# Kernel tuning notes

Measured on AMD Instinct MI355X. Metric: run time of the kernel, lower is better.

Reference implementation:

```python
import jax, jax.numpy as jnp
import numpy as np

EPS = 1e-12  # torch F.normalize eps

def _l2norm(v, axis):
    return v / jnp.maximum(jnp.linalg.norm(v, axis=axis, keepdims=True), EPS)

def setup_inputs() -> dict:
    key = jax.random.key(0)
    k1, k2, k3 = jax.random.split(key, 3)
    N, C, H, W, K = 128, 64, 64, 64, 100
    ALPHA = 100.0
    x = jax.random.normal(k1, (N, C, H, W), dtype=jnp.float32)
    # centroids initialized as F.normalize(rand(K, C)) per __init__
    centroids = jax.random.uniform(k2, (K, C), dtype=jnp.float32)
    centroids = _l2norm(centroids, axis=1)
    # _init_params ties conv weight/bias to centroids (random=False)
    conv_w = 2.0 * ALPHA * centroids                      # [K, C] (1x1 conv kernel)
    conv_b = -ALPHA * jnp.linalg.norm(centroids, axis=1)  # [K]
    return {"x": x, "conv_w": conv_w, "conv_b": conv_b, "centroids": centroids}

def reference(x, conv_w, conv_b, centroids):
    N, C, H, W = x.shape
    K = centroids.shape[0]
    xf = x.reshape(N, C, H * W)                      # [N, C, L]
    # get_assignments: L2-normalize over channels (local copy only)
    x_hat = _l2norm(xf, axis=1)
    logits = jnp.einsum('kc,ncl->nkl', conv_w, x_hat) + conv_b[None, :, None]
    a = jax.nn.softmax(logits, axis=1)               # soft assignment over K
    # residual sum over L expressed as matmul (same math as expand-subtract-sum):
    # vlad[n,k,c] = sum_l a[n,k,l]*xf[n,c,l] - centroids[k,c]*sum_l a[n,k,l]
    agg = jnp.einsum('nkl,ncl->nkc', a, xf)          # note: un-normalized xf, per original code
    vlad = agg - centroids[None] * jnp.sum(a, axis=-1)[..., None]
    # build_vlad (random=False): intra-normalize per cluster, flatten, L2-normalize
    vlad = _l2norm(vlad, axis=2)
    vlad = vlad.reshape(N, K * C)
    vlad = _l2norm(vlad, axis=1)
    # Wrapper applies a final F.normalize (idempotent here but kept for faithfulness)
    vlad = _l2norm(vlad, axis=1)
    return vlad
```

## Files before the change

### kernel.cpp

```cpp
#include <hip/hip_runtime.h>
#include <hip/hip_bf16.h>
#include <cstdint>

#define NB   128
#define CD   64
#define LD   4096
#define KC   100
#define KT   7
#define KR   (KT * 16)
#define AKP  72
#define LSPLIT 8
#define LCH  (LD / LSPLIT)
#define ITERS (LCH / 64)

typedef __attribute__((ext_vector_type(8))) short bf16x8;
typedef __attribute__((ext_vector_type(4))) float f32x4;

__device__ __forceinline__ short bfbits(float f) {
    __hip_bfloat16 h = __float2bfloat16(f);
    return *reinterpret_cast<short*>(&h);
}
__device__ __forceinline__ float bffloat(short s) {
    __hip_bfloat16 h = *reinterpret_cast<__hip_bfloat16*>(&s);
    return __bfloat162float(h);
}

__global__ void k_prep(const float* __restrict__ w, const float* __restrict__ b,
                       uint4* __restrict__ wfrag, float* __restrict__ b_pad)
{
    const int tid = threadIdx.x;
    if (tid < 128) b_pad[tid] = (tid < KC) ? b[tid] : -1e30f;
    if (tid < 64) {
        const int r16 = tid & 15, gg = tid >> 4;
        for (int t = 0; t < KT; ++t) {
            const int k = t * 16 + r16;
            for (int h = 0; h < 2; ++h) {
                short hi8[8], lo8[8];
                for (int j = 0; j < 8; ++j) {
                    const int c = h * 32 + gg * 8 + j;
                    float v = (k < KC) ? w[k * CD + c] : 0.f;
                    short hb = bfbits(v);
                    hi8[j] = hb;
                    lo8[j] = bfbits(v - bffloat(hb));
                }
                wfrag[((t * 2 + h) * 2 + 0) * 64 + tid] = *reinterpret_cast<uint4*>(hi8);
                wfrag[((t * 2 + h) * 2 + 1) * 64 + tid] = *reinterpret_cast<uint4*>(lo8);
            }
        }
    }
}

__global__ __launch_bounds__(256, 3) void k_fused(
    const float* __restrict__ x, const uint4* __restrict__ wfrag,
    const float* __restrict__ b_pad,
    float* __restrict__ agg_pT, float* __restrict__ asum_pT, int n0)
{
    __shared__ __align__(16) __hip_bfloat16 akl[KR][AKP];
    __shared__ __align__(16) uint4 wlds[KT * 2 * 2 * 64];

    const int tid  = threadIdx.x;
    const int lane = tid & 63;
    const int wv   = tid >> 6;
    const int lloc = lane & 15;
    const int g    = lane >> 4;

    for (int i = tid; i < KT * 2 * 2 * 64; i += 256) wlds[i] = wfrag[i];

    const int nn = blockIdx.x >> 3;
    const int ls = blockIdx.x & 7;
    const int n  = n0 + nn;
    const float* xb = x + (size_t)n * CD * LD + ls * LCH;

    const float4* bp4 = reinterpret_cast<const float4*>(b_pad);
    float4 bv[KT];
#pragma unroll
    for (int t = 0; t < KT; ++t) bv[t] = bp4[t * 4 + g];

    f32x4 aagg[KT];
#pragma unroll
    for (int mt = 0; mt < KT; ++mt) aagg[mt] = (f32x4){0.f, 0.f, 0.f, 0.f};
    float asl = 0.f;

    const bf16x8* wfp = reinterpret_cast<const bf16x8*>(wlds);
    const int lw = wv * 16 + lloc;
    const int cb = wv * 16 + lloc;

    __syncthreads();

    for (int it = 0; it < ITERS; ++it) {
        const float* xcol = xb + it * 64 + lw;
        float ss = 0.f;
        bf16x8 bhi0, blo0, bhi1, blo1;
#pragma unroll
        for (int j = 0; j < 8; ++j) {
            float v0 = xcol[(size_t)(g * 8 + j) * LD];
            ss = fmaf(v0, v0, ss);
            short h0 = bfbits(v0);
            bhi0[j] = h0; blo0[j] = bfbits(v0 - bffloat(h0));
            float v1 = xcol[(size_t)(32 + g * 8 + j) * LD];
            ss = fmaf(v1, v1, ss);
            short h1 = bfbits(v1);
            bhi1[j] = h1; blo1[j] = bfbits(v1 - bffloat(h1));
        }
        ss += __shfl_xor(ss, 16);
        ss += __shfl_xor(ss, 32);
        const float rn = 1.0f / fmaxf(sqrtf(ss), 1e-12f);

        f32x4 acc[KT];
#pragma unroll
        for (int t = 0; t < KT; ++t) acc[t] = (f32x4){0.f, 0.f, 0.f, 0.f};
#pragma unroll
        for (int t = 0; t < KT; ++t) {
            bf16x8 wh0 = wfp[((t * 2 + 0) * 2 + 0) * 64 + lane];
            bf16x8 wl0 = wfp[((t * 2 + 0) * 2 + 1) * 64 + lane];
            bf16x8 wh1 = wfp[((t * 2 + 1) * 2 + 0) * 64 + lane];
            bf16x8 wl1 = wfp[((t * 2 + 1) * 2 + 1) * 64 + lane];
            acc[t] = __builtin_amdgcn_mfma_f32_16x16x32_bf16(wh0, bhi0, acc[t], 0, 0, 0);
            acc[t] = __builtin_amdgcn_mfma_f32_16x16x32_bf16(wh1, bhi1, acc[t], 0, 0, 0);
            acc[t] = __builtin_amdgcn_mfma_f32_16x16x32_bf16(wh0, blo0, acc[t], 0, 0, 0);
            acc[t] = __builtin_amdgcn_mfma_f32_16x16x32_bf16(wh1, blo1, acc[t], 0, 0, 0);
            acc[t] = __builtin_amdgcn_mfma_f32_16x16x32_bf16(wl0, bhi0, acc[t], 0, 0, 0);
            acc[t] = __builtin_amdgcn_mfma_f32_16x16x32_bf16(wl1, bhi1, acc[t], 0, 0, 0);
        }

        float m = -3.0e38f;
#pragma unroll
        for (int t = 0; t < KT; ++t) {
            acc[t][0] = fmaf(acc[t][0], rn, bv[t].x);
            acc[t][1] = fmaf(acc[t][1], rn, bv[t].y);
            acc[t][2] = fmaf(acc[t][2], rn, bv[t].z);
            acc[t][3] = fmaf(acc[t][3], rn, bv[t].w);
            m = fmaxf(m, fmaxf(fmaxf(acc[t][0], acc[t][1]), fmaxf(acc[t][2], acc[t][3])));
        }
        m = fmaxf(m, __shfl_xor(m, 16));
        m = fmaxf(m, __shfl_xor(m, 32));
        float s = 0.f;
#pragma unroll
        for (int t = 0; t < KT; ++t) {
#pragma unroll
            for (int r = 0; r < 4; ++r) {
                float e = __expf(acc[t][r] - m);
                acc[t][r] = e;
                s += e;
            }
        }
        s += __shfl_xor(s, 16);
        s += __shfl_xor(s, 32);
        const float inv = 1.0f / s;

        __syncthreads();

#pragma unroll
        for (int r = 0; r < 4; ++r) {
#pragma unroll
            for (int t = 0; t < KT; ++t)
                akl[t * 16 + g * 4 + r][lw] = __float2bfloat16(acc[t][r] * inv);
        }
        __syncthreads();

        if (tid < KR) {
            const bf16x8* rp = reinterpret_cast<const bf16x8*>(&akl[tid][0]);
            float rs = 0.f;
#pragma unroll
            for (int q = 0; q < 8; ++q) {
                bf16x8 v = rp[q];
#pragma unroll
                for (int j = 0; j < 8; ++j) rs += bffloat(v[j]);
            }
            asl += rs;
        }

#pragma unroll
        for (int h = 0; h < 2; ++h) {
            const float* xrow = xb + (size_t)cb * LD + it * 64 + h * 32 + g * 8;
            float4 xr0 = *reinterpret_cast<const float4*>(xrow);
            float4 xr1 = *reinterpret_cast<const float4*>(xrow + 4);
            float xv8[8] = {xr0.x, xr0.y, xr0.z, xr0.w, xr1.x, xr1.y, xr1.z, xr1.w};
            bf16x8 xh, xl;
#pragma unroll
            for (int j = 0; j < 8; ++j) {
                float v = xv8[j];
                short hb = bfbits(v);
                xh[j] = hb; xl[j] = bfbits(v - bffloat(hb));
            }
#pragma unroll
            for (int mt = 0; mt < KT; ++mt) {
                bf16x8 af = *reinterpret_cast<const bf16x8*>(
                    &akl[mt * 16 + lloc][h * 32 + g * 8]);
                aagg[mt] = __builtin_amdgcn_mfma_f32_16x16x32_bf16(af, xh, aagg[mt], 0, 0, 0);
                aagg[mt] = __builtin_amdgcn_mfma_f32_16x16x32_bf16(af, xl, aagg[mt], 0, 0, 0);
            }
        }
    }

    const size_t nls = (size_t)nn * LSPLIT + ls;
    float* ap = agg_pT + (nls * 64 + cb) * 128 + g * 4;
#pragma unroll
    for (int mt = 0; mt < KT; ++mt)
        *reinterpret_cast<f32x4*>(ap + mt * 16) = aagg[mt];
    if (tid < KR) asum_pT[nls * KR + tid] = asl;
}

__global__ __launch_bounds__(256, 1) void k_final(
    const float* __restrict__ agg_pT, const float* __restrict__ asum_pT,
    const float* __restrict__ cent, float* __restrict__ out, int n0)
{
    __shared__ float vbuf[KC][65];
    __shared__ float asum_s[KR];
    __shared__ float rn_s[KC];
    __shared__ float red[256];

    const int tid = threadIdx.x;
    const int nn  = blockIdx.x;
    const int n   = n0 + nn;
    const size_t nb8 = (size_t)nn * LSPLIT;

    if (tid < KR) {
        float s = 0.f;
#pragma unroll
        for (int ls = 0; ls < LSPLIT; ++ls)
            s += asum_pT[(nb8 + ls) * KR + tid];
        asum_s[tid] = s;
    }
    __syncthreads();

    for (int idx = tid; idx < 64 * 128; idx += 256) {
        int c = idx >> 7, k = idx & 127;
        if (k < KC) {
            float s = 0.f;
#pragma unroll
            for (int ls = 0; ls < LSPLIT; ++ls)
                s += agg_pT[((nb8 + ls) * 64 + c) * 128 + k];
            vbuf[k][c] = fmaf(-cent[k * CD + c], asum_s[k], s);
        }
    }
    __syncthreads();

    if (tid < KC) {
        float ssq = 0.f;
#pragma unroll 8
        for (int c = 0; c < CD; ++c) {
            float v = vbuf[tid][c];
            ssq = fmaf(v, v, ssq);
        }
        rn_s[tid] = 1.0f / fmaxf(sqrtf(ssq), 1e-12f);
    }
    __syncthreads();

    float gp = 0.f;
    for (int idx = tid; idx < KC * CD; idx += 256) {
        int k = idx >> 6, c = idx & 63;
        float v = vbuf[k][c] * rn_s[k];
        gp = fmaf(v, v, gp);
    }
    red[tid] = gp;
    __syncthreads();
    for (int off = 128; off > 0; off >>= 1) {
        if (tid < off) red[tid] += red[tid + off];
        __syncthreads();
    }
    const float gnorm = 1.0f / fmaxf(sqrtf(red[0]), 1e-12f);

    float* op = out + (size_t)n * (KC * CD);
    for (int idx = tid; idx < KC * CD; idx += 256) {
        int k = idx >> 6, c = idx & 63;
        op[idx] = vbuf[k][c] * rn_s[k] * gnorm;
    }
}

extern "C" void kernel_launch(void* const* d_in, const int* in_sizes, int n_in,
                              void* d_out, int out_size, void* d_ws, size_t ws_size,
                              hipStream_t stream)
{
    const float* x  = (const float*)d_in[0];
    const float* w  = (const float*)d_in[1];
    const float* b  = (const float*)d_in[2];
    const float* ct = (const float*)d_in[3];
    float* out = (float*)d_out;

    char* wsp = (char*)d_ws;
    uint4* wfrag = (uint4*)wsp;
    float* b_pad = (float*)(wsp + 28672);
    char* chunk  = wsp + 32768;

    const size_t agg_per_n  = (size_t)LSPLIT * 64 * 128 * 4;
    const size_t asum_per_n = (size_t)LSPLIT * KR * 4;
    const size_t per_n = agg_per_n + asum_per_n;

    size_t avail = ws_size > 32768 ? ws_size - 32768 : 0;
    int nc = (int)(avail / per_n);
    if (nc < 1) nc = 1;
    if (nc > NB) nc = NB;

    float* agg_pT  = (float*)chunk;
    float* asum_pT = (float*)(chunk + agg_per_n * (size_t)nc);

    k_prep<<<1, 128, 0, stream>>>(w, b, wfrag, b_pad);
    for (int n0 = 0; n0 < NB; n0 += nc) {
        int cn = NB - n0; if (cn > nc) cn = nc;
        k_fused<<<cn * LSPLIT, 256, 0, stream>>>(x, wfrag, b_pad, agg_pT, asum_pT, n0);
        k_final<<<cn, 256, 0, stream>>>(agg_pT, asum_pT, ct, out, n0);
    }
}
```

Baseline: 100.1 us.

## Prefetch next x tiles into registers and accumulate assignment sums in registers

Software-pipelines the global loads of x: the column and row fragments for the next 64-wide L chunk are issued into registers while the current chunk's softmax and aggregation MFMAs run. The per-iteration shared-memory row-sum of the assignment tile, done by a subset of threads, is replaced by per-lane fp32 partial sums reduced with shuffles and shared memory once at the end. Bias values are reloaded from global each iteration instead of held in registers to offset the extra prefetch registers. Register pressure rises under the 3-blocks-per-SM launch bound, which risks spills or lower occupancy. The assignment sums now come from fp32 values rather than the bf16-rounded tile, which slightly changes numerics.

```diff
diff --git a/kernel.cpp b/kernel.cpp
--- a/kernel.cpp
+++ b/kernel.cpp
@@ -57,6 +57,7 @@
 {
     __shared__ __align__(16) __hip_bfloat16 akl[KR][AKP];
     __shared__ __align__(16) uint4 wlds[KT * 2 * 2 * 64];
+    __shared__ float asum_sm[4][KR];
 
     const int tid  = threadIdx.x;
     const int lane = tid & 63;
@@ -72,32 +73,48 @@
     const float* xb = x + (size_t)n * CD * LD + ls * LCH;
 
     const float4* bp4 = reinterpret_cast<const float4*>(b_pad);
-    float4 bv[KT];
-#pragma unroll
-    for (int t = 0; t < KT; ++t) bv[t] = bp4[t * 4 + g];
 
     f32x4 aagg[KT];
 #pragma unroll
     for (int mt = 0; mt < KT; ++mt) aagg[mt] = (f32x4){0.f, 0.f, 0.f, 0.f};
-    float asl = 0.f;
+    float pasum[KT][4];
+#pragma unroll
+    for (int t = 0; t < KT; ++t)
+#pragma unroll
+        for (int r = 0; r < 4; ++r) pasum[t][r] = 0.f;
 
     const bf16x8* wfp = reinterpret_cast<const bf16x8*>(wlds);
     const int lw = wv * 16 + lloc;
     const int cb = wv * 16 + lloc;
 
+    float pvc[16];
+    float4 pvr0, pvr1, pvr2, pvr3;
+    {
+        const float* xcol = xb + lw;
+#pragma unroll
+        for (int j = 0; j < 8; ++j) {
+            pvc[j]     = xcol[(size_t)(g * 8 + j) * LD];
+            pvc[8 + j] = xcol[(size_t)(32 + g * 8 + j) * LD];
+        }
+        const float* xrow = xb + (size_t)cb * LD + g * 8;
+        pvr0 = *reinterpret_cast<const float4*>(xrow);
+        pvr1 = *reinterpret_cast<const float4*>(xrow + 4);
+        pvr2 = *reinterpret_cast<const float4*>(xrow + 32);
+        pvr3 = *reinterpret_cast<const float4*>(xrow + 36);
+    }
+
     __syncthreads();
 
     for (int it = 0; it < ITERS; ++it) {
-        const float* xcol = xb + it * 64 + lw;
         float ss = 0.f;
         bf16x8 bhi0, blo0, bhi1, blo1;
 #pragma unroll
         for (int j = 0; j < 8; ++j) {
-            float v0 = xcol[(size_t)(g * 8 + j) * LD];
+            float v0 = pvc[j];
             ss = fmaf(v0, v0, ss);
             short h0 = bfbits(v0);
             bhi0[j] = h0; blo0[j] = bfbits(v0 - bffloat(h0));
-            float v1 = xcol[(size_t)(32 + g * 8 + j) * LD];
+            float v1 = pvc[8 + j];
             ss = fmaf(v1, v1, ss);
             short h1 = bfbits(v1);
             bhi1[j] = h1; blo1[j] = bfbits(v1 - bffloat(h1));
@@ -126,10 +143,11 @@
         float m = -3.0e38f;
 #pragma unroll
         for (int t = 0; t < KT; ++t) {
-            acc[t][0] = fmaf(acc[t][0], rn, bv[t].x);
-            acc[t][1] = fmaf(acc[t][1], rn, bv[t].y);
-            acc[t][2] = fmaf(acc[t][2], rn, bv[t].z);
-            acc[t][3] = fmaf(acc[t][3], rn, bv[t].w);
+            float4 bt = bp4[t * 4 + g];
+            acc[t][0] = fmaf(acc[t][0], rn, bt.x);
+            acc[t][1] = fmaf(acc[t][1], rn, bt.y);
+            acc[t][2] = fmaf(acc[t][2], rn, bt.z);
+            acc[t][3] = fmaf(acc[t][3], rn, bt.w);
             m = fmaxf(m, fmaxf(fmaxf(acc[t][0], acc[t][1]), fmaxf(acc[t][2], acc[t][3])));
         }
         m = fmaxf(m, __shfl_xor(m, 16));
@@ -147,6 +165,14 @@
         s += __shfl_xor(s, 16);
         s += __shfl_xor(s, 32);
         const float inv = 1.0f / s;
+#pragma unroll
+        for (int t = 0; t < KT; ++t) {
+#pragma unroll
+            for (int r = 0; r < 4; ++r) {
+                acc[t][r] *= inv;
+                pasum[t][r] += acc[t][r];
+            }
+        }
 
         __syncthreads();
 
@@ -154,51 +180,73 @@
         for (int r = 0; r < 4; ++r) {
 #pragma unroll
             for (int t = 0; t < KT; ++t)
-                akl[t * 16 + g * 4 + r][lw] = __float2bfloat16(acc[t][r] * inv);
-        }
+                akl[t * 16 + g * 4 + r][lw] = __float2bfloat16(acc[t][r]);
+        }
+
+        if (it + 1 < ITERS) {
+            const float* xcol = xb + (it + 1) * 64 + lw;
+#pragma unroll
+            for (int j = 0; j < 8; ++j) {
+                pvc[j]     = xcol[(size_t)(g * 8 + j) * LD];
+                pvc[8 + j] = xcol[(size_t)(32 + g * 8 + j) * LD];
+            }
+        }
+
         __syncthreads();
 
-        if (tid < KR) {
-            const bf16x8* rp = reinterpret_cast<const bf16x8*>(&akl[tid][0]);
-            float rs = 0.f;
-#pragma unroll
-            for (int q = 0; q < 8; ++q) {
-                bf16x8 v = rp[q];
-#pragma unroll
-                for (int j = 0; j < 8; ++j) rs += bffloat(v[j]);
-            }
-            asl += rs;
-        }
-
-#pragma unroll
-        for (int h = 0; h < 2; ++h) {
-            const float* xrow = xb + (size_t)cb * LD + it * 64 + h * 32 + g * 8;
-            float4 xr0 = *reinterpret_cast<const float4*>(xrow);
-            float4 xr1 = *reinterpret_cast<const float4*>(xrow + 4);
-            float xv8[8] = {xr0.x, xr0.y, xr0.z, xr0.w, xr1.x, xr1.y, xr1.z, xr1.w};
-            bf16x8 xh, xl;
+        bf16x8 xh0, xl0, xh1, xl1;
+        {
+            float xv0[8] = {pvr0.x, pvr0.y, pvr0.z, pvr0.w, pvr1.x, pvr1.y, pvr1.z, pvr1.w};
+            float xv1[8] = {pvr2.x, pvr2.y, pvr2.z, pvr2.w, pvr3.x, pvr3.y, pvr3.z, pvr3.w};
 #pragma unroll
             for (int j = 0; j < 8; ++j) {
-                float v = xv8[j];
-                short hb = bfbits(v);
-                xh[j] = hb; xl[j] = bfbits(v - bffloat(hb));
-            }
-#pragma unroll
-            for (int mt = 0; mt < KT; ++mt) {
-                bf16x8 af = *reinterpret_cast<const bf16x8*>(
-                    &akl[mt * 16 + lloc][h * 32 + g * 8]);
-                aagg[mt] = __builtin_amdgcn_mfma_f32_16x16x32_bf16(af, xh, aagg[mt], 0, 0, 0);
-                aagg[mt] = __builtin_amdgcn_mfma_f32_16x16x32_bf16(af, xl, aagg[mt], 0, 0, 0);
-            }
-        }
-    }
+                short hb0 = bfbits(xv0[j]);
+                xh0[j] = hb0; xl0[j] = bfbits(xv0[j] - bffloat(hb0));
+                short hb1 = bfbits(xv1[j]);
+                xh1[j] = hb1; xl1[j] = bfbits(xv1[j] - bffloat(hb1));
+            }
+        }
+        if (it + 1 < ITERS) {
+            const float* xrow = xb + (size_t)cb * LD + (it + 1) * 64 + g * 8;
+            pvr0 = *reinterpret_cast<const float4*>(xrow);
+            pvr1 = *reinterpret_cast<const float4*>(xrow + 4);
+            pvr2 = *reinterpret_cast<const float4*>(xrow + 32);
+            pvr3 = *reinterpret_cast<const float4*>(xrow + 36);
+        }
+#pragma unroll
+        for (int mt = 0; mt < KT; ++mt) {
+            bf16x8 af0 = *reinterpret_cast<const bf16x8*>(&akl[mt * 16 + lloc][g * 8]);
+            aagg[mt] = __builtin_amdgcn_mfma_f32_16x16x32_bf16(af0, xh0, aagg[mt], 0, 0, 0);
+            aagg[mt] = __builtin_amdgcn_mfma_f32_16x16x32_bf16(af0, xl0, aagg[mt], 0, 0, 0);
+            bf16x8 af1 = *reinterpret_cast<const bf16x8*>(&akl[mt * 16 + lloc][32 + g * 8]);
+            aagg[mt] = __builtin_amdgcn_mfma_f32_16x16x32_bf16(af1, xh1, aagg[mt], 0, 0, 0);
+            aagg[mt] = __builtin_amdgcn_mfma_f32_16x16x32_bf16(af1, xl1, aagg[mt], 0, 0, 0);
+        }
+    }
+
+#pragma unroll
+    for (int t = 0; t < KT; ++t) {
+#pragma unroll
+        for (int r = 0; r < 4; ++r) {
+            float v = pasum[t][r];
+            v += __shfl_xor(v, 1);
+            v += __shfl_xor(v, 2);
+            v += __shfl_xor(v, 4);
+            v += __shfl_xor(v, 8);
+            if (lloc == 0) asum_sm[wv][t * 16 + g * 4 + r] = v;
+        }
+    }
+    __syncthreads();
 
     const size_t nls = (size_t)nn * LSPLIT + ls;
+    if (tid < KR)
+        asum_pT[nls * KR + tid] = asum_sm[0][tid] + asum_sm[1][tid]
+                                + asum_sm[2][tid] + asum_sm[3][tid];
+
     float* ap = agg_pT + (nls * 64 + cb) * 128 + g * 4;
 #pragma unroll
     for (int mt = 0; mt < KT; ++mt)
         *reinterpret_cast<f32x4*>(ap + mt * 16) = aagg[mt];
-    if (tid < KR) asum_pT[nls * KR + tid] = asl;
 }
 
 __global__ __launch_bounds__(256, 1) void k_final(
```

New measurement: 106.5 us. +6.4%, slower.

## Keep softmax probabilities in registers and feed aggregation MFMA directly, removing LDS staging

Applied to the files above, without the earlier changes.

The logits MFMA now has its operands swapped so each lane's accumulator already holds the layout needed as the A operand of an f16 16x16x16 MFMA for aggregation. This removes the per-iteration LDS write and read of the assignment matrix along with its two barriers. Each wave now keeps a partial 112x64 aggregate (28 f32x4 accumulators), and the waves are summed through LDS at the end with the output layout transposed to k-major. The cost is much higher register pressure (launch bounds drop from 3 to 2 blocks), softmax reductions that need more shuffles, and probabilities rounded to fp16 instead of bf16.

```diff
diff --git a/kernel.cpp b/kernel.cpp
--- a/kernel.cpp
+++ b/kernel.cpp
@@ -8,13 +8,13 @@
 #define KC   100
 #define KT   7
 #define KR   (KT * 16)
-#define AKP  72
 #define LSPLIT 8
 #define LCH  (LD / LSPLIT)
 #define ITERS (LCH / 64)
 
 typedef __attribute__((ext_vector_type(8))) short bf16x8;
 typedef __attribute__((ext_vector_type(4))) float f32x4;
+typedef __attribute__((ext_vector_type(4))) _Float16 f16x4;
 
 __device__ __forceinline__ short bfbits(float f) {
     __hip_bfloat16 h = __float2bfloat16(f);
@@ -50,13 +50,13 @@
     }
 }
 
-__global__ __launch_bounds__(256, 3) void k_fused(
+__global__ __launch_bounds__(256, 2) void k_fused(
     const float* __restrict__ x, const uint4* __restrict__ wfrag,
     const float* __restrict__ b_pad,
     float* __restrict__ agg_pT, float* __restrict__ asum_pT, int n0)
 {
-    __shared__ __align__(16) __hip_bfloat16 akl[KR][AKP];
     __shared__ __align__(16) uint4 wlds[KT * 2 * 2 * 64];
+    __shared__ float asum_sm[4][KR];
 
     const int tid  = threadIdx.x;
     const int lane = tid & 63;
@@ -71,40 +71,58 @@
     const int n  = n0 + nn;
     const float* xb = x + (size_t)n * CD * LD + ls * LCH;
 
-    const float4* bp4 = reinterpret_cast<const float4*>(b_pad);
-    float4 bv[KT];
-#pragma unroll
-    for (int t = 0; t < KT; ++t) bv[t] = bp4[t * 4 + g];
-
-    f32x4 aagg[KT];
-#pragma unroll
-    for (int mt = 0; mt < KT; ++mt) aagg[mt] = (f32x4){0.f, 0.f, 0.f, 0.f};
-    float asl = 0.f;
+    float bv7[KT];
+#pragma unroll
+    for (int t = 0; t < KT; ++t) bv7[t] = b_pad[t * 16 + lloc];
+
+    f32x4 aagg[KT][4];
+#pragma unroll
+    for (int t = 0; t < KT; ++t)
+#pragma unroll
+        for (int ct = 0; ct < 4; ++ct) aagg[t][ct] = (f32x4){0.f, 0.f, 0.f, 0.f};
+    float pasum[KT];
+#pragma unroll
+    for (int t = 0; t < KT; ++t) pasum[t] = 0.f;
 
     const bf16x8* wfp = reinterpret_cast<const bf16x8*>(wlds);
     const int lw = wv * 16 + lloc;
-    const int cb = wv * 16 + lloc;
 
     __syncthreads();
 
     for (int it = 0; it < ITERS; ++it) {
-        const float* xcol = xb + it * 64 + lw;
+        const int lb = it * 64;
+
+        float pvc[16];
+#pragma unroll
+        for (int j = 0; j < 8; ++j) {
+            pvc[j]     = xb[(size_t)(g * 8 + j) * LD + lb + lw];
+            pvc[8 + j] = xb[(size_t)(32 + g * 8 + j) * LD + lb + lw];
+        }
+        float4 xv4[4];
+        const float* xt = xb + lb + wv * 16 + g * 4;
+#pragma unroll
+        for (int ct = 0; ct < 4; ++ct)
+            xv4[ct] = *reinterpret_cast<const float4*>(xt + (size_t)(ct * 16 + lloc) * LD);
+
         float ss = 0.f;
-        bf16x8 bhi0, blo0, bhi1, blo1;
+        bf16x8 xhi0, xlo0, xhi1, xlo1;
 #pragma unroll
         for (int j = 0; j < 8; ++j) {
-            float v0 = xcol[(size_t)(g * 8 + j) * LD];
+            float v0 = pvc[j];
             ss = fmaf(v0, v0, ss);
             short h0 = bfbits(v0);
-            bhi0[j] = h0; blo0[j] = bfbits(v0 - bffloat(h0));
-            float v1 = xcol[(size_t)(32 + g * 8 + j) * LD];
+            xhi0[j] = h0; xlo0[j] = bfbits(v0 - bffloat(h0));
+            float v1 = pvc[8 + j];
             ss = fmaf(v1, v1, ss);
             short h1 = bfbits(v1);
-            bhi1[j] = h1; blo1[j] = bfbits(v1 - bffloat(h1));
+            xhi1[j] = h1; xlo1[j] = bfbits(v1 - bffloat(h1));
         }
         ss += __shfl_xor(ss, 16);
         ss += __shfl_xor(ss, 32);
-        const float rn = 1.0f / fmaxf(sqrtf(ss), 1e-12f);
+        const float rnl = 1.0f / fmaxf(sqrtf(ss), 1e-12f);
+        float rnr[4];
+#pragma unroll
+        for (int r = 0; r < 4; ++r) rnr[r] = __shfl(rnl, g * 4 + r, 16);
 
         f32x4 acc[KT];
 #pragma unroll
@@ -115,90 +133,115 @@
             bf16x8 wl0 = wfp[((t * 2 + 0) * 2 + 1) * 64 + lane];
             bf16x8 wh1 = wfp[((t * 2 + 1) * 2 + 0) * 64 + lane];
             bf16x8 wl1 = wfp[((t * 2 + 1) * 2 + 1) * 64 + lane];
-            acc[t] = __builtin_amdgcn_mfma_f32_16x16x32_bf16(wh0, bhi0, acc[t], 0, 0, 0);
-            acc[t] = __builtin_amdgcn_mfma_f32_16x16x32_bf16(wh1, bhi1, acc[t], 0, 0, 0);
-            acc[t] = __builtin_amdgcn_mfma_f32_16x16x32_bf16(wh0, blo0, acc[t], 0, 0, 0);
-            acc[t] = __builtin_amdgcn_mfma_f32_16x16x32_bf16(wh1, blo1, acc[t], 0, 0, 0);
-            acc[t] = __builtin_amdgcn_mfma_f32_16x16x32_bf16(wl0, bhi0, acc[t], 0, 0, 0);
-            acc[t] = __builtin_amdgcn_mfma_f32_16x16x32_bf16(wl1, bhi1, acc[t], 0, 0, 0);
-        }
-
-        float m = -3.0e38f;
-#pragma unroll
-        for (int t = 0; t < KT; ++t) {
-            acc[t][0] = fmaf(acc[t][0], rn, bv[t].x);
-            acc[t][1] = fmaf(acc[t][1], rn, bv[t].y);
-            acc[t][2] = fmaf(acc[t][2], rn, bv[t].z);
-            acc[t][3] = fmaf(acc[t][3], rn, bv[t].w);
-            m = fmaxf(m, fmaxf(fmaxf(acc[t][0], acc[t][1]), fmaxf(acc[t][2], acc[t][3])));
-        }
-        m = fmaxf(m, __shfl_xor(m, 16));
-        m = fmaxf(m, __shfl_xor(m, 32));
-        float s = 0.f;
+            acc[t] = __builtin_amdgcn_mfma_f32_16x16x32_bf16(xhi0, wh0, acc[t], 0, 0, 0);
+            acc[t] = __builtin_amdgcn_mfma_f32_16x16x32_bf16(xhi1, wh1, acc[t], 0, 0, 0);
+            acc[t] = __builtin_amdgcn_mfma_f32_16x16x32_bf16(xlo0, wh0, acc[t], 0, 0, 0);
+            acc[t] = __builtin_amdgcn_mfma_f32_16x16x32_bf16(xlo1, wh1, acc[t], 0, 0, 0);
+            acc[t] = __builtin_amdgcn_mfma_f32_16x16x32_bf16(xhi0, wl0, acc[t], 0, 0, 0);
+            acc[t] = __builtin_amdgcn_mfma_f32_16x16x32_bf16(xhi1, wl1, acc[t], 0, 0, 0);
+        }
+
+        float mr[4] = {-3.0e38f, -3.0e38f, -3.0e38f, -3.0e38f};
 #pragma unroll
         for (int t = 0; t < KT; ++t) {
 #pragma unroll
             for (int r = 0; r < 4; ++r) {
-                float e = __expf(acc[t][r] - m);
+                acc[t][r] = fmaf(acc[t][r], rnr[r], bv7[t]);
+                mr[r] = fmaxf(mr[r], acc[t][r]);
+            }
+        }
+#pragma unroll
+        for (int r = 0; r < 4; ++r) {
+            mr[r] = fmaxf(mr[r], __shfl_xor(mr[r], 1));
+            mr[r] = fmaxf(mr[r], __shfl_xor(mr[r], 2));
+            mr[r] = fmaxf(mr[r], __shfl_xor(mr[r], 4));
+            mr[r] = fmaxf(mr[r], __shfl_xor(mr[r], 8));
+        }
+        float sr[4] = {0.f, 0.f, 0.f, 0.f};
+#pragma unroll
+        for (int t = 0; t < KT; ++t) {
+#pragma unroll
+            for (int r = 0; r < 4; ++r) {
+                float e = __expf(acc[t][r] - mr[r]);
                 acc[t][r] = e;
-                s += e;
-            }
-        }
-        s += __shfl_xor(s, 16);
-        s += __shfl_xor(s, 32);
-        const float inv = 1.0f / s;
-
+                sr[r] += e;
+            }
+        }
+#pragma unroll
+        for (int r = 0; r < 4; ++r) {
+            sr[r] += __shfl_xor(sr[r], 1);
+            sr[r] += __shfl_xor(sr[r], 2);
+            sr[r] += __shfl_xor(sr[r], 4);
+            sr[r] += __shfl_xor(sr[r], 8);
+            sr[r] = 1.0f / sr[r];
+        }
+
+        f16x4 pa[KT];
+#pragma unroll
+        for (int t = 0; t < KT; ++t) {
+            float a0 = acc[t][0] * sr[0];
+            float a1 = acc[t][1] * sr[1];
+            float a2 = acc[t][2] * sr[2];
+            float a3 = acc[t][3] * sr[3];
+            pasum[t] += (a0 + a1) + (a2 + a3);
+            pa[t][0] = (_Float16)a0; pa[t][1] = (_Float16)a1;
+            pa[t][2] = (_Float16)a2; pa[t][3] = (_Float16)a3;
+        }
+
+        f16x4 xh4[4], xl4[4];
+#pragma unroll
+        for (int ct = 0; ct < 4; ++ct) {
+            float vv[4] = {xv4[ct].x, xv4[ct].y, xv4[ct].z, xv4[ct].w};
+#pragma unroll
+            for (int j = 0; j < 4; ++j) {
+                _Float16 h = (_Float16)vv[j];
+                xh4[ct][j] = h;
+                xl4[ct][j] = (_Float16)(vv[j] - (float)h);
+            }
+        }
+
+#pragma unroll
+        for (int t = 0; t < KT; ++t)
+#pragma unroll
+            for (int ct = 0; ct < 4; ++ct) {
+                aagg[t][ct] = __builtin_amdgcn_mfma_f32_16x16x16f16(pa[t], xh4[ct], aagg[t][ct], 0, 0, 0);
+                aagg[t][ct] = __builtin_amdgcn_mfma_f32_16x16x16f16(pa[t], xl4[ct], aagg[t][ct], 0, 0, 0);
+            }
+    }
+
+#pragma unroll
+    for (int t = 0; t < KT; ++t) {
+        float v = pasum[t];
+        v += __shfl_xor(v, 16);
+        v += __shfl_xor(v, 32);
+        if (g == 0) asum_sm[wv][t * 16 + lloc] = v;
+    }
+    __syncthreads();
+
+    const size_t nls = (size_t)nn * LSPLIT + ls;
+    if (tid < KR)
+        asum_pT[nls * KR + tid] = asum_sm[0][tid] + asum_sm[1][tid]
+                                + asum_sm[2][tid] + asum_sm[3][tid];
+
+    float* red = reinterpret_cast<float*>(wlds);
+#define RED(w, k, c) red[(((w) * 16 + (k)) * 65) + (c)]
+    for (int t = 0; t < KT; ++t) {
+        if (t) __syncthreads();
+#pragma unroll
+        for (int ct = 0; ct < 4; ++ct)
+#pragma unroll
+            for (int rg = 0; rg < 4; ++rg)
+                RED(wv, g * 4 + rg, ct * 16 + lloc) = aagg[t][ct][rg];
         __syncthreads();
-
-#pragma unroll
-        for (int r = 0; r < 4; ++r) {
-#pragma unroll
-            for (int t = 0; t < KT; ++t)
-                akl[t * 16 + g * 4 + r][lw] = __float2bfloat16(acc[t][r] * inv);
-        }
-        __syncthreads();
-
-        if (tid < KR) {
-            const bf16x8* rp = reinterpret_cast<const bf16x8*>(&akl[tid][0]);
-            float rs = 0.f;
-#pragma unroll
-            for (int q = 0; q < 8; ++q) {
-                bf16x8 v = rp[q];
-#pragma unroll
-                for (int j = 0; j < 8; ++j) rs += bffloat(v[j]);
-            }
-            asl += rs;
-        }
-
-#pragma unroll
-        for (int h = 0; h < 2; ++h) {
-            const float* xrow = xb + (size_t)cb * LD + it * 64 + h * 32 + g * 8;
-            float4 xr0 = *reinterpret_cast<const float4*>(xrow);
-            float4 xr1 = *reinterpret_cast<const float4*>(xrow + 4);
-            float xv8[8] = {xr0.x, xr0.y, xr0.z, xr0.w, xr1.x, xr1.y, xr1.z, xr1.w};
-            bf16x8 xh, xl;
-#pragma unroll
-            for (int j = 0; j < 8; ++j) {
-                float v = xv8[j];
-                short hb = bfbits(v);
-                xh[j] = hb; xl[j] = bfbits(v - bffloat(hb));
-            }
-#pragma unroll
-            for (int mt = 0; mt < KT; ++mt) {
-                bf16x8 af = *reinterpret_cast<const bf16x8*>(
-                    &akl[mt * 16 + lloc][h * 32 + g * 8]);
-                aagg[mt] = __builtin_amdgcn_mfma_f32_16x16x32_bf16(af, xh, aagg[mt], 0, 0, 0);
-                aagg[mt] = __builtin_amdgcn_mfma_f32_16x16x32_bf16(af, xl, aagg[mt], 0, 0, 0);
-            }
-        }
-    }
-
-    const size_t nls = (size_t)nn * LSPLIT + ls;
-    float* ap = agg_pT + (nls * 64 + cb) * 128 + g * 4;
-#pragma unroll
-    for (int mt = 0; mt < KT; ++mt)
-        *reinterpret_cast<f32x4*>(ap + mt * 16) = aagg[mt];
-    if (tid < KR) asum_pT[nls * KR + tid] = asl;
+        const int kk = tid >> 4, c0 = (tid & 15) * 4;
+        f32x4 v;
+#pragma unroll
+        for (int q = 0; q < 4; ++q)
+            v[q] = RED(0, kk, c0 + q) + RED(1, kk, c0 + q)
+                 + RED(2, kk, c0 + q) + RED(3, kk, c0 + q);
+        *reinterpret_cast<f32x4*>(agg_pT + ((nls * 128 + t * 16 + kk) * 64 + c0)) = v;
+    }
+#undef RED
 }
 
 __global__ __launch_bounds__(256, 1) void k_final(
@@ -224,13 +267,13 @@
     }
     __syncthreads();
 
-    for (int idx = tid; idx < 64 * 128; idx += 256) {
-        int c = idx >> 7, k = idx & 127;
+    for (int idx = tid; idx < 128 * 64; idx += 256) {
+        int k = idx >> 6, c = idx & 63;
         if (k < KC) {
             float s = 0.f;
 #pragma unroll
             for (int ls = 0; ls < LSPLIT; ++ls)
-                s += agg_pT[((nb8 + ls) * 64 + c) * 128 + k];
+                s += agg_pT[((nb8 + ls) * 128 + k) * 64 + c];
             vbuf[k][c] = fmaf(-cent[k * CD + c], asum_s[k], s);
         }
     }
@@ -283,7 +326,7 @@
     float* b_pad = (float*)(wsp + 28672);
     char* chunk  = wsp + 32768;
 
-    const size_t agg_per_n  = (size_t)LSPLIT * 64 * 128 * 4;
+    const size_t agg_per_n  = (size_t)LSPLIT * 128 * 64 * 4;
     const size_t asum_per_n = (size_t)LSPLIT * KR * 4;
     const size_t per_n = agg_per_n + asum_per_n;
 
```

After: 242.3 us. +142.1%, slower.
